# Kernel optimization log

Measured on AMD Instinct MI355X. Metric: run time of the kernel, lower is better.

The kernel has to match this reference:

```python
import jax, jax.numpy as jnp
import numpy as np

B, S, HID = 1, 2048, 4096
NH, NKV, HD = 32, 8, 128
GROUPS = NH // NKV
SCALING = HD ** -0.5


def approx_matmul(a, b):
    # BaselineApproxMatmulFP16: matmul performed in fp16 precision
    return jnp.matmul(a.astype(jnp.float16), b.astype(jnp.float16)).astype(a.dtype)


def rotate_half(x):
    x1, x2 = jnp.split(x, 2, axis=-1)
    return jnp.concatenate([-x2, x1], axis=-1)


def setup_inputs() -> dict:
    key = jax.random.key(0)
    ks = jax.random.split(key, 6)
    hidden_states = jax.random.normal(ks[0], (B, S, HID), jnp.float32)
    # Proper RoPE tables (HF llama convention: freqs duplicated across halves)
    inv_freq = 1.0 / (10000.0 ** (jnp.arange(0, HD, 2, dtype=jnp.float32) / HD))
    t = jnp.arange(S, dtype=jnp.float32)
    freqs = jnp.outer(t, inv_freq)                      # [S, HD/2]
    emb = jnp.concatenate([freqs, freqs], axis=-1)      # [S, HD]
    cos = jnp.cos(emb)[None]                            # [B, S, HD]
    sin = jnp.sin(emb)[None]
    # Additive causal mask [B,1,S,S]
    causal = jnp.triu(jnp.full((S, S), -1e9, jnp.float32), k=1)[None, None]
    scale = 0.02
    wq = jax.random.normal(ks[1], (HID, NH * HD), jnp.float32) * scale
    wk = jax.random.normal(ks[2], (HID, NKV * HD), jnp.float32) * scale
    wv = jax.random.normal(ks[3], (HID, NKV * HD), jnp.float32) * scale
    wo = jax.random.normal(ks[4], (NH * HD, HID), jnp.float32) * scale
    return {"hidden_states": hidden_states, "cos": cos, "sin": sin,
            "attn_mask": causal, "wq": wq, "wk": wk, "wv": wv, "wo": wo}


def reference(hidden_states, cos, sin, attn_mask, wq, wk, wv, wo):
    x = hidden_states
    # projections -> [B, heads, S, HD]
    q = (x @ wq).reshape(B, S, NH, HD).transpose(0, 2, 1, 3)
    k = (x @ wk).reshape(B, S, NKV, HD).transpose(0, 2, 1, 3)
    v = (x @ wv).reshape(B, S, NKV, HD).transpose(0, 2, 1, 3)
    # RoPE
    c = cos[:, None]  # [B,1,S,HD]
    s = sin[:, None]
    q = q * c + rotate_half(q) * s
    k = k * c + rotate_half(k) * s
    # repeat_kv (GQA): [B,NKV,S,HD] -> [B,NH,S,HD]
    k = jnp.repeat(k, GROUPS, axis=1)
    v = jnp.repeat(v, GROUPS, axis=1)
    # eager attention with fp16 approx matmul
    attn = approx_matmul(q, k.transpose(0, 1, 3, 2)) * SCALING  # [B,NH,S,S]
    attn = attn + attn_mask
    attn = jax.nn.softmax(attn.astype(jnp.float32), axis=-1).astype(q.dtype)
    out = approx_matmul(attn, v)                                # [B,NH,S,HD]
    out = out.transpose(0, 2, 1, 3).reshape(B, S, NH * HD)
    return out @ wo
```

## Files before the change

### kernel.cpp

```cpp
#include <hip/hip_runtime.h>
#include <hip/hip_bf16.h>
#include <hip/hip_fp16.h>

typedef _Float16 half8 __attribute__((ext_vector_type(8)));
typedef _Float16 half4 __attribute__((ext_vector_type(4)));
typedef float f32x4 __attribute__((ext_vector_type(4)));
typedef unsigned int u32;

#define S_LEN 2048
#define HID_DIM 4096
#define N_HEADS 32
#define N_KV 8
#define HEAD_DIM 128
#define SCALE_QK 0.08838834764831845f

__device__ __forceinline__ void async16(void* lds, const void* gptr) {
  __builtin_amdgcn_global_load_lds(
      (const __attribute__((address_space(1))) u32*)gptr,
      (__attribute__((address_space(3))) u32*)lds, 16, 0, 0);
}

__device__ __forceinline__ void transpose_tile(const float* __restrict__ src,
                                               _Float16* __restrict__ dst, int R, int C,
                                               int bx, int by, float (*tile)[73], int t) {
  {
    const int c4 = (t & 15) * 4;
    const int r0 = t >> 4;
#pragma unroll
    for (int i = 0; i < 4; i++) {
      int r = r0 + 16 * i;
      float4 v = *(const float4*)&src[(long)(by * 64 + r) * C + bx * 64 + c4];
      tile[r][c4] = v.x; tile[r][c4 + 1] = v.y; tile[r][c4 + 2] = v.z; tile[r][c4 + 3] = v.w;
    }
  }
  __syncthreads();
  const int kc = t & 7;
  const int n0 = t >> 3;
#pragma unroll
  for (int p = 0; p < 2; p++) {
    int n = n0 + 32 * p;
    half8 o;
#pragma unroll
    for (int j = 0; j < 8; j++) o[j] = (_Float16)tile[kc * 8 + j][n];
    *(half8*)&dst[(long)(bx * 64 + n) * R + by * 64 + kc * 8] = o;
  }
}

__global__ void prep_kernel(const float* __restrict__ x, _Float16* __restrict__ Xh,
                            const float* __restrict__ wq, _Float16* __restrict__ WqT,
                            const float* __restrict__ wk, const float* __restrict__ wv,
                            _Float16* __restrict__ WkvT) {
  __shared__ float tile[64][73];
  const int bid = blockIdx.x;
  const int t = threadIdx.x;
  if (bid < 4096) {
    int i = bid * 256 + t;
    float4 a = ((const float4*)x)[2 * i];
    float4 b = ((const float4*)x)[2 * i + 1];
    half8 h;
    h[0] = (_Float16)a.x; h[1] = (_Float16)a.y; h[2] = (_Float16)a.z; h[3] = (_Float16)a.w;
    h[4] = (_Float16)b.x; h[5] = (_Float16)b.y; h[6] = (_Float16)b.z; h[7] = (_Float16)b.w;
    ((half8*)Xh)[i] = h;
  } else if (bid < 8192) {
    int tt = bid - 4096;
    transpose_tile(wq, WqT, 4096, 4096, tt & 63, tt >> 6, tile, t);
  } else if (bid < 9216) {
    int tt = bid - 8192;
    transpose_tile(wk, WkvT, 4096, 1024, tt & 15, tt >> 4, tile, t);
  } else {
    int tt = bid - 9216;
    transpose_tile(wv, WkvT + (size_t)1024 * 4096, 4096, 1024, tt & 15, tt >> 4, tile, t);
  }
}

template <int NHEADS>
__global__ void rope_tiled(_Float16* __restrict__ t, const float* __restrict__ cosb,
                           const float* __restrict__ sinb) {
  int idx = blockIdx.x * 256 + threadIdx.x;
  int slo = idx & 15;
  int d8 = (idx >> 4) & 7;
  int h = (idx >> 7) % NHEADS;
  int s16 = idx / (128 * NHEADS);
  int s = s16 * 16 + slo;
  int d0 = d8 * 8;
  long c0 = (long)(h * 128 + s16) * 4;
  long base = (c0 + (d0 >> 5)) * 512 + ((d0 >> 3) & 3) * 128 + slo * 8;
  half8 a = *(half8*)(t + base);
  half8 b = *(half8*)(t + base + 1024);
  const float* cp = cosb + s * 128 + d0;
  const float* sp = sinb + s * 128 + d0;
  half8 olo, ohi;
#pragma unroll
  for (int j = 0; j < 8; j++) {
    float c = cp[j], sn = sp[j];
    float av = (float)a[j], bv = (float)b[j];
    olo[j] = (_Float16)(av * c - bv * sn);
    ohi[j] = (_Float16)(bv * c + av * sn);
  }
  *(half8*)(t + base) = olo;
  *(half8*)(t + base + 1024) = ohi;
}

__global__ __launch_bounds__(256, 3) void gemm_qkv(
    const _Float16* __restrict__ A, const _Float16* __restrict__ BtQ,
    const _Float16* __restrict__ BtKV, _Float16* __restrict__ Qt,
    _Float16* __restrict__ Kt, _Float16* __restrict__ Vt) {
  __shared__ _Float16 As[128 * 64];
  __shared__ _Float16 Bs[128 * 64];
  const int K = 4096;
  const int tid = threadIdx.x, lane = tid & 63, wid = tid >> 6;
  const int row0 = blockIdx.y * 128;
  const int col0 = blockIdx.x * 128;
  const int wm = wid >> 1, wn = wid & 1;
  const int lr = lane & 15, lg = lane >> 4;

  const _Float16* bbase = (col0 < 4096) ? (BtQ + (long)col0 * K)
                                        : (BtKV + (long)(col0 - 4096) * K);
  const int scol = ((lane & 7) ^ ((lane >> 3) & 7)) * 8;
  const _Float16* aptr = A + (long)(row0 + wid * 32 + (lane >> 3)) * K + scol;
  const _Float16* bptr = bbase + (long)(wid * 32 + (lane >> 3)) * K + scol;
  _Float16* alds = As + (wid * 4) * 512;
  _Float16* blds = Bs + (wid * 4) * 512;

  f32x4 acc[4][4] = {};
  for (int k0 = 0; k0 < K; k0 += 64) {
#pragma unroll
    for (int j = 0; j < 4; j++) {
      async16(alds + j * 512, aptr + k0 + (long)j * 8 * K);
      async16(blds + j * 512, bptr + k0 + (long)j * 8 * K);
    }
    __syncthreads();
    half8 a[2][4], b[2][4];
#pragma unroll
    for (int kk = 0; kk < 2; kk++)
#pragma unroll
      for (int mf = 0; mf < 4; mf++) {
        a[kk][mf] = *(const half8*)&As[(wm * 64 + mf * 16 + lr) * 64 +
                                       (((kk * 4 + lg) ^ (lr & 7)) * 8)];
        b[kk][mf] = *(const half8*)&Bs[(wn * 64 + mf * 16 + lr) * 64 +
                                       (((kk * 4 + lg) ^ (lr & 7)) * 8)];
      }
#pragma unroll
    for (int kk = 0; kk < 2; kk++)
#pragma unroll
      for (int mf = 0; mf < 4; mf++)
#pragma unroll
        for (int nf = 0; nf < 4; nf++)
          acc[mf][nf] =
              __builtin_amdgcn_mfma_f32_16x16x32_f16(a[kk][mf], b[kk][nf], acc[mf][nf], 0, 0, 0);
    __syncthreads();
  }

#pragma unroll
  for (int mf = 0; mf < 4; mf++) {
#pragma unroll
    for (int nf = 0; nf < 4; nf++) {
      int rbase = row0 + wm * 64 + mf * 16 + lg * 4;
      int col = col0 + wn * 64 + nf * 16 + lr;
      if (col0 < 4096) {
        int h = col >> 7, d = col & 127;
        long off = ((long)((h * 128 + (rbase >> 4)) * 4 + (d >> 5))) * 512 +
                   ((d >> 3) & 3) * 128 + (rbase & 15) * 8 + (d & 7);
#pragma unroll
        for (int i = 0; i < 4; i++) Qt[off + i * 8] = (_Float16)acc[mf][nf][i];
      } else if (col0 < 5120) {
        int gc = col - 4096;
        int g = gc >> 7, d = gc & 127;
        long off = ((long)((g * 128 + (rbase >> 4)) * 4 + (d >> 5))) * 512 +
                   ((d >> 3) & 3) * 128 + (rbase & 15) * 8 + (d & 7);
#pragma unroll
        for (int i = 0; i < 4; i++) Kt[off + i * 8] = (_Float16)acc[mf][nf][i];
      } else {
        int gc = col - 5120;
        int gq = gc >> 7, d = gc & 127;
        int dt = d >> 4, lrr = d & 15;
        int kvb = rbase >> 5, lgv = (rbase >> 3) & 3, j = rbase & 7;
        half4 v;
#pragma unroll
        for (int i = 0; i < 4; i++) v[i] = (_Float16)acc[mf][nf][i];
        long off = ((long)(gq * 64 + kvb) * 8 + dt) * 512 + (lgv * 16 + lrr) * 8 + j;
        *(half4*)&Vt[off] = v;
      }
    }
  }
}

__global__ __launch_bounds__(256, 3) void gemm_out(
    const _Float16* __restrict__ A, const _Float16* __restrict__ Bt,
    float* __restrict__ C) {
  __shared__ _Float16 As[128 * 64];
  __shared__ _Float16 Bs[128 * 64];
  const int K = 4096;
  const int tid = threadIdx.x, lane = tid & 63, wid = tid >> 6;
  const int row0 = blockIdx.y * 128;
  const int col0 = blockIdx.x * 128;
  const int wm = wid >> 1, wn = wid & 1;
  const int lr = lane & 15, lg = lane >> 4;

  const int scol = ((lane & 7) ^ ((lane >> 3) & 7)) * 8;
  const _Float16* aptr = A + (long)(row0 + wid * 32 + (lane >> 3)) * K + scol;
  const _Float16* bptr = Bt + (long)(col0 + wid * 32 + (lane >> 3)) * K + scol;
  _Float16* alds = As + (wid * 4) * 512;
  _Float16* blds = Bs + (wid * 4) * 512;

  f32x4 acc[4][4] = {};
  for (int k0 = 0; k0 < K; k0 += 64) {
#pragma unroll
    for (int j = 0; j < 4; j++) {
      async16(alds + j * 512, aptr + k0 + (long)j * 8 * K);
      async16(blds + j * 512, bptr + k0 + (long)j * 8 * K);
    }
    __syncthreads();
    half8 a[2][4], b[2][4];
#pragma unroll
    for (int kk = 0; kk < 2; kk++)
#pragma unroll
      for (int mf = 0; mf < 4; mf++) {
        a[kk][mf] = *(const half8*)&As[(wm * 64 + mf * 16 + lr) * 64 +
                                       (((kk * 4 + lg) ^ (lr & 7)) * 8)];
        b[kk][mf] = *(const half8*)&Bs[(wn * 64 + mf * 16 + lr) * 64 +
                                       (((kk * 4 + lg) ^ (lr & 7)) * 8)];
      }
#pragma unroll
    for (int kk = 0; kk < 2; kk++)
#pragma unroll
      for (int mf = 0; mf < 4; mf++)
#pragma unroll
        for (int nf = 0; nf < 4; nf++)
          acc[mf][nf] =
              __builtin_amdgcn_mfma_f32_16x16x32_f16(a[kk][mf], b[kk][nf], acc[mf][nf], 0, 0, 0);
    __syncthreads();
  }
#pragma unroll
  for (int mf = 0; mf < 4; mf++)
#pragma unroll
    for (int nf = 0; nf < 4; nf++) {
      int rbase = row0 + wm * 64 + mf * 16 + lg * 4;
      int col = col0 + wn * 64 + nf * 16 + lr;
#pragma unroll
      for (int i = 0; i < 4; i++)
        C[(long)(rbase + i) * 4096 + col] = acc[mf][nf][i];
    }
}

__global__ __launch_bounds__(256, 3) void attn_wo_kernel(
    const _Float16* __restrict__ Qt, const _Float16* __restrict__ Kt,
    const _Float16* __restrict__ Vt, _Float16* __restrict__ O,
    const float* __restrict__ cosb, const float* __restrict__ sinb,
    const float* __restrict__ wo, _Float16* __restrict__ WoT) {
  __shared__ __align__(16) char smem[36864];
  const int tid = threadIdx.x;
  const int bid = blockIdx.x;

  if (bid >= 1024) {
    int tt = bid - 1024;
    transpose_tile(wo, WoT, 4096, 4096, tt & 63, tt >> 6, (float(*)[73])smem, tid);
    return;
  }

  _Float16* Kb = (_Float16*)smem;
  _Float16* Vb = (_Float16*)(smem + 16384);
  _Float16* Pb = (_Float16*)(smem + 32768) + (tid >> 6) * 512;

  const int lane = tid & 63;
  const int wid = tid >> 6;
  const int g = bid & 7;
  const int qidx = bid >> 3;
  const int qt16 = (qidx < 64) ? (2 * qidx) : (2 * (127 - qidx) + 1);
  const int h = g * 4 + wid;
  const int qrow0 = qt16 * 16;
  const int ntiles = (qrow0 + 47) >> 5;
  const int lr = lane & 15;
  const int lg = lane >> 4;

  half8 qf[4];
  {
    const _Float16* qp = Qt + ((long)(h * 128 + qt16) * 4) * 512 + lane * 8;
#pragma unroll
    for (int t = 0; t < 4; t++) qf[t] = *(const half8*)(qp + t * 512);
    int s = qrow0 + lr;
#pragma unroll
    for (int t = 0; t < 2; t++) {
      const float* cp = cosb + s * 128 + t * 32 + lg * 8;
      const float* sp = sinb + s * 128 + t * 32 + lg * 8;
#pragma unroll
      for (int j = 0; j < 8; j++) {
        float c = cp[j], sn = sp[j];
        float lo = (float)qf[t][j], hi = (float)qf[t + 2][j];
        qf[t][j]     = (_Float16)(lo * c - hi * sn);
        qf[t + 2][j] = (_Float16)(hi * c + lo * sn);
      }
    }
  }

  const _Float16* kgb = Kt + (long)g * 128 * 2048 + lane * 8;
  const _Float16* vgb = Vt + (long)g * 64 * 4096 + lane * 8;

  {
    async16(&Kb[(2 * wid) * 512], kgb + (2 * wid) * 512);
    async16(&Kb[(2 * wid + 1) * 512], kgb + (2 * wid + 1) * 512);
    async16(&Vb[(2 * wid) * 512], vgb + (2 * wid) * 512);
    async16(&Vb[(2 * wid + 1) * 512], vgb + (2 * wid + 1) * 512);
  }
  __syncthreads();

  f32x4 oacc[8] = {};
  float mrow[4] = {-1e30f, -1e30f, -1e30f, -1e30f};
  float lsum[4] = {0.f, 0.f, 0.f, 0.f};

  for (int t = 0; t < ntiles; t++) {
    const int kb = t * 32;
    const int cur = t & 1;
    if (t + 1 < ntiles) {
      const _Float16* ks = kgb + (long)(t + 1) * 4096;
      const _Float16* vs = vgb + (long)(t + 1) * 4096;
      async16(&Kb[(cur ^ 1) * 4096 + (2 * wid) * 512], ks + (2 * wid) * 512);
      async16(&Kb[(cur ^ 1) * 4096 + (2 * wid + 1) * 512], ks + (2 * wid + 1) * 512);
      async16(&Vb[(cur ^ 1) * 4096 + (2 * wid) * 512], vs + (2 * wid) * 512);
      async16(&Vb[(cur ^ 1) * 4096 + (2 * wid + 1) * 512], vs + (2 * wid + 1) * 512);
    }

    half8 kf[8];
#pragma unroll
    for (int c = 0; c < 8; c++)
      kf[c] = *(const half8*)&Kb[cur * 4096 + c * 512 + lane * 8];
    half8 vf[8];
#pragma unroll
    for (int dt = 0; dt < 8; dt++)
      vf[dt] = *(const half8*)&Vb[cur * 4096 + dt * 512 + lane * 8];

    f32x4 sacc[2] = {};
    __builtin_amdgcn_s_setprio(1);
#pragma unroll
    for (int s = 0; s < 2; s++)
#pragma unroll
      for (int t2 = 0; t2 < 4; t2++)
        sacc[s] = __builtin_amdgcn_mfma_f32_16x16x32_f16(qf[t2], kf[s * 4 + t2], sacc[s], 0, 0, 0);
    __builtin_amdgcn_s_setprio(0);

    float mx[4];
    bool grow = false;
#pragma unroll
    for (int i = 0; i < 4; i++) {
      int qrow = qrow0 + lg * 4 + i;
      float s0 = sacc[0][i] * SCALE_QK;
      float s1 = sacc[1][i] * SCALE_QK;
      if (kb + lr > qrow) s0 = -1e30f;
      if (kb + 16 + lr > qrow) s1 = -1e30f;
      sacc[0][i] = s0; sacc[1][i] = s1;
      mx[i] = fmaxf(s0, s1);
      grow |= (mx[i] > mrow[i] + 4.0f);
    }
    if (__any((int)grow)) {
#pragma unroll
      for (int i = 0; i < 4; i++) {
        float m = mx[i];
        m = fmaxf(m, __shfl_xor(m, 1));
        m = fmaxf(m, __shfl_xor(m, 2));
        m = fmaxf(m, __shfl_xor(m, 4));
        m = fmaxf(m, __shfl_xor(m, 8));
        float mn = fmaxf(mrow[i], m);
        float scl = __expf(mrow[i] - mn);
        mrow[i] = mn;
        lsum[i] *= scl;
#pragma unroll
        for (int dt = 0; dt < 8; dt++) oacc[dt][i] *= scl;
      }
    }
    float p[2][4];
#pragma unroll
    for (int i = 0; i < 4; i++) {
      p[0][i] = __expf(sacc[0][i] - mrow[i]);
      p[1][i] = __expf(sacc[1][i] - mrow[i]);
      lsum[i] += p[0][i] + p[1][i];
    }

#pragma unroll
    for (int sub = 0; sub < 2; sub++)
#pragma unroll
      for (int i = 0; i < 4; i++)
        Pb[(lg * 4 + i) * 32 + sub * 16 + lr] = (_Float16)p[sub][i];
    half8 pa = *(const half8*)&Pb[lr * 32 + lg * 8];

    __builtin_amdgcn_s_setprio(1);
#pragma unroll
    for (int dt = 0; dt < 8; dt++)
      oacc[dt] = __builtin_amdgcn_mfma_f32_16x16x32_f16(pa, vf[dt], oacc[dt], 0, 0, 0);
    __builtin_amdgcn_s_setprio(0);

    __syncthreads();
  }

#pragma unroll
  for (int i = 0; i < 4; i++) {
    float t2 = lsum[i];
    t2 += __shfl_xor(t2, 1);
    t2 += __shfl_xor(t2, 2);
    t2 += __shfl_xor(t2, 4);
    t2 += __shfl_xor(t2, 8);
    lsum[i] = t2;
  }
#pragma unroll
  for (int dt = 0; dt < 8; dt++) {
#pragma unroll
    for (int i = 0; i < 4; i++) {
      float o = oacc[dt][i] / lsum[i];
      O[(long)(qrow0 + lg * 4 + i) * HID_DIM + h * HEAD_DIM + dt * 16 + lr] = (_Float16)o;
    }
  }
}

extern "C" void kernel_launch(void* const* d_in, const int* in_sizes, int n_in,
                              void* d_out, int out_size, void* d_ws, size_t ws_size,
                              hipStream_t stream) {
  const float* x    = (const float*)d_in[0];
  const float* cosb = (const float*)d_in[1];
  const float* sinb = (const float*)d_in[2];
  const float* wq = (const float*)d_in[4];
  const float* wk = (const float*)d_in[5];
  const float* wv = (const float*)d_in[6];
  const float* wo = (const float*)d_in[7];
  float* out = (float*)d_out;

  char* ws = (char*)d_ws;
  _Float16* Xh    = (_Float16*)(ws);
  _Float16* Oattn = Xh;
  _Float16* Qt    = (_Float16*)(ws + (size_t)(16 << 20));
  _Float16* Kt    = (_Float16*)(ws + (size_t)(32 << 20));
  _Float16* Vt    = (_Float16*)(ws + (size_t)(36 << 20));
  _Float16* WqT   = (_Float16*)(ws + (size_t)(40 << 20));
  _Float16* WoT   = WqT;
  _Float16* WkvT  = (_Float16*)d_out;

  dim3 b256(256);

  prep_kernel<<<dim3(10240), b256, 0, stream>>>(x, Xh, wq, WqT, wk, wv, WkvT);

  gemm_qkv<<<dim3(6144 / 128, S_LEN / 128), b256, 0, stream>>>(Xh, WqT, WkvT, Qt, Kt, Vt);

  rope_tiled<N_KV><<<dim3(N_KV * 16384 / 256), b256, 0, stream>>>(Kt, cosb, sinb);

  attn_wo_kernel<<<dim3(1024 + 4096), b256, 0, stream>>>(Qt, Kt, Vt, Oattn, cosb, sinb, wo, WoT);

  gemm_out<<<dim3(4096 / 128, S_LEN / 128), b256, 0, stream>>>(Oattn, WoT, out);
}
```

Measured before the change: 296.7 us.

## Fuse K RoPE into QKV GEMM epilogue and skip causal mask on off-diagonal tiles

Drops the separate rope_tiled launch for K. The QKV GEMM epilogue now applies rotary embedding to K tiles, with the upper-half accumulators exchanged between warps through a padded LDS buffer, which grows shared memory to 34 KB. In the attention loop, causal masking now runs only on the last (diagonal) tile instead of every tile. This saves a kernel launch, a read-write pass over K and per-tile compare work, at the cost of an extra barrier and LDS traffic in the K epilogue, plus possibly lower occupancy.

```diff
diff --git a/kernel.cpp b/kernel.cpp
--- a/kernel.cpp
+++ b/kernel.cpp
@@ -73,40 +73,14 @@
   }
 }
 
-template <int NHEADS>
-__global__ void rope_tiled(_Float16* __restrict__ t, const float* __restrict__ cosb,
-                           const float* __restrict__ sinb) {
-  int idx = blockIdx.x * 256 + threadIdx.x;
-  int slo = idx & 15;
-  int d8 = (idx >> 4) & 7;
-  int h = (idx >> 7) % NHEADS;
-  int s16 = idx / (128 * NHEADS);
-  int s = s16 * 16 + slo;
-  int d0 = d8 * 8;
-  long c0 = (long)(h * 128 + s16) * 4;
-  long base = (c0 + (d0 >> 5)) * 512 + ((d0 >> 3) & 3) * 128 + slo * 8;
-  half8 a = *(half8*)(t + base);
-  half8 b = *(half8*)(t + base + 1024);
-  const float* cp = cosb + s * 128 + d0;
-  const float* sp = sinb + s * 128 + d0;
-  half8 olo, ohi;
-#pragma unroll
-  for (int j = 0; j < 8; j++) {
-    float c = cp[j], sn = sp[j];
-    float av = (float)a[j], bv = (float)b[j];
-    olo[j] = (_Float16)(av * c - bv * sn);
-    ohi[j] = (_Float16)(bv * c + av * sn);
-  }
-  *(half8*)(t + base) = olo;
-  *(half8*)(t + base + 1024) = ohi;
-}
-
 __global__ __launch_bounds__(256, 3) void gemm_qkv(
     const _Float16* __restrict__ A, const _Float16* __restrict__ BtQ,
     const _Float16* __restrict__ BtKV, _Float16* __restrict__ Qt,
-    _Float16* __restrict__ Kt, _Float16* __restrict__ Vt) {
-  __shared__ _Float16 As[128 * 64];
-  __shared__ _Float16 Bs[128 * 64];
+    _Float16* __restrict__ Kt, _Float16* __restrict__ Vt,
+    const float* __restrict__ cosb, const float* __restrict__ sinb) {
+  __shared__ __align__(16) char smem[34816];
+  _Float16* As = (_Float16*)smem;
+  _Float16* Bs = (_Float16*)(smem + 16384);
   const int K = 4096;
   const int tid = threadIdx.x, lane = tid & 63, wid = tid >> 6;
   const int row0 = blockIdx.y * 128;
@@ -151,26 +125,59 @@
     __syncthreads();
   }
 
-#pragma unroll
-  for (int mf = 0; mf < 4; mf++) {
-#pragma unroll
-    for (int nf = 0; nf < 4; nf++) {
-      int rbase = row0 + wm * 64 + mf * 16 + lg * 4;
-      int col = col0 + wn * 64 + nf * 16 + lr;
-      if (col0 < 4096) {
+  if (col0 < 4096) {
+#pragma unroll
+    for (int mf = 0; mf < 4; mf++)
+#pragma unroll
+      for (int nf = 0; nf < 4; nf++) {
+        int rbase = row0 + wm * 64 + mf * 16 + lg * 4;
+        int col = col0 + wn * 64 + nf * 16 + lr;
         int h = col >> 7, d = col & 127;
         long off = ((long)((h * 128 + (rbase >> 4)) * 4 + (d >> 5))) * 512 +
                    ((d >> 3) & 3) * 128 + (rbase & 15) * 8 + (d & 7);
 #pragma unroll
         for (int i = 0; i < 4; i++) Qt[off + i * 8] = (_Float16)acc[mf][nf][i];
-      } else if (col0 < 5120) {
-        int gc = col - 4096;
-        int g = gc >> 7, d = gc & 127;
-        long off = ((long)((g * 128 + (rbase >> 4)) * 4 + (d >> 5))) * 512 +
-                   ((d >> 3) & 3) * 128 + (rbase & 15) * 8 + (d & 7);
-#pragma unroll
-        for (int i = 0; i < 4; i++) Kt[off + i * 8] = (_Float16)acc[mf][nf][i];
-      } else {
+      }
+  } else if (col0 < 5120) {
+    const int g = (col0 - 4096) >> 7;
+    float* fl = (float*)smem;
+    if (wn == 1) {
+#pragma unroll
+      for (int mf = 0; mf < 4; mf++)
+#pragma unroll
+        for (int nf = 0; nf < 4; nf++)
+#pragma unroll
+          for (int i = 0; i < 4; i++)
+            fl[(wm * 64 + mf * 16 + lg * 4 + i) * 68 + nf * 16 + lr] = acc[mf][nf][i];
+    }
+    __syncthreads();
+    if (wn == 0) {
+#pragma unroll
+      for (int mf = 0; mf < 4; mf++)
+#pragma unroll
+        for (int nf = 0; nf < 4; nf++)
+#pragma unroll
+          for (int i = 0; i < 4; i++) {
+            int s_local = wm * 64 + mf * 16 + lg * 4 + i;
+            int d = nf * 16 + lr;
+            int s_glob = row0 + s_local;
+            float lo = acc[mf][nf][i];
+            float hi = fl[s_local * 68 + d];
+            float c = cosb[s_glob * 128 + d];
+            float sn = sinb[s_glob * 128 + d];
+            long off = ((long)((g * 128 + (s_glob >> 4)) * 4 + (d >> 5))) * 512 +
+                       ((d >> 3) & 3) * 128 + (s_glob & 15) * 8 + (d & 7);
+            Kt[off] = (_Float16)(lo * c - hi * sn);
+            Kt[off + 1024] = (_Float16)(hi * c + lo * sn);
+          }
+    }
+  } else {
+#pragma unroll
+    for (int mf = 0; mf < 4; mf++)
+#pragma unroll
+      for (int nf = 0; nf < 4; nf++) {
+        int rbase = row0 + wm * 64 + mf * 16 + lg * 4;
+        int col = col0 + wn * 64 + nf * 16 + lr;
         int gc = col - 5120;
         int gq = gc >> 7, d = gc & 127;
         int dt = d >> 4, lrr = d & 15;
@@ -181,7 +188,6 @@
         long off = ((long)(gq * 64 + kvb) * 8 + dt) * 512 + (lgv * 16 + lrr) * 8 + j;
         *(half4*)&Vt[off] = v;
       }
-    }
   }
 }
 
@@ -338,17 +344,24 @@
         sacc[s] = __builtin_amdgcn_mfma_f32_16x16x32_f16(qf[t2], kf[s * 4 + t2], sacc[s], 0, 0, 0);
     __builtin_amdgcn_s_setprio(0);
 
+#pragma unroll
+    for (int i = 0; i < 4; i++) {
+      sacc[0][i] *= SCALE_QK;
+      sacc[1][i] *= SCALE_QK;
+    }
+    if (t == ntiles - 1) {
+#pragma unroll
+      for (int i = 0; i < 4; i++) {
+        int qrow = qrow0 + lg * 4 + i;
+        if (kb + lr > qrow) sacc[0][i] = -1e30f;
+        if (kb + 16 + lr > qrow) sacc[1][i] = -1e30f;
+      }
+    }
     float mx[4];
     bool grow = false;
 #pragma unroll
     for (int i = 0; i < 4; i++) {
-      int qrow = qrow0 + lg * 4 + i;
-      float s0 = sacc[0][i] * SCALE_QK;
-      float s1 = sacc[1][i] * SCALE_QK;
-      if (kb + lr > qrow) s0 = -1e30f;
-      if (kb + 16 + lr > qrow) s1 = -1e30f;
-      sacc[0][i] = s0; sacc[1][i] = s1;
-      mx[i] = fmaxf(s0, s1);
+      mx[i] = fmaxf(sacc[0][i], sacc[1][i]);
       grow |= (mx[i] > mrow[i] + 4.0f);
     }
     if (__any((int)grow)) {
@@ -436,9 +449,8 @@
 
   prep_kernel<<<dim3(10240), b256, 0, stream>>>(x, Xh, wq, WqT, wk, wv, WkvT);
 
-  gemm_qkv<<<dim3(6144 / 128, S_LEN / 128), b256, 0, stream>>>(Xh, WqT, WkvT, Qt, Kt, Vt);
-
-  rope_tiled<N_KV><<<dim3(N_KV * 16384 / 256), b256, 0, stream>>>(Kt, cosb, sinb);
+  gemm_qkv<<<dim3(6144 / 128, S_LEN / 128), b256, 0, stream>>>(Xh, WqT, WkvT, Qt, Kt, Vt,
+                                                               cosb, sinb);
 
   attn_wo_kernel<<<dim3(1024 + 4096), b256, 0, stream>>>(Qt, Kt, Vt, Oattn, cosb, sinb, wo, WoT);
 
```

New measurement: 290.9 us (median of 2 runs). No clear change (-2.0%).
